# Optimization experiments

Hardware: AMD Instinct MI355X
Metric: run time of the kernel (lower is better)

## Reference

```python
import jax, jax.numpy as jnp
import numpy as np

M, K, D = 8, 4096, 128
N, H, W = 8, 64, 64


def setup_inputs() -> dict:
    key = jax.random.key(0)
    k1, k2, k3, k4 = jax.random.split(key, 4)
    codes = jax.random.randint(k1, (N, H, W, M), 0, K, dtype=jnp.int64)
    codebook = jax.random.normal(k2, (M, K, D), dtype=jnp.float32)
    wq = jax.random.normal(k3, (M, D, D), dtype=jnp.float32) / jnp.sqrt(jnp.float32(D))
    bq = jax.random.normal(k4, (M, D), dtype=jnp.float32) * 0.01
    return {"codes": codes, "codebook": codebook, "wq": wq, "bq": bq}


def reference(codes, codebook, wq, bq):
    n, h, w, m = codes.shape
    # gather: indexed[n,h,w,m,d] = codebook[m_idx, codes[n,h,w,m_idx]]
    ix = jnp.arange(m)  # broadcasts against codes' last dim
    indexed = codebook[ix, codes]  # [n,h,w,m,d]
    # per-group small matmul + bias
    out = jnp.einsum('nhwmd,mcd->nhwmc', indexed, wq) + bq  # [n,h,w,m,d]
    return out.reshape(n, h, w, -1).transpose(0, 3, 1, 2)  # [n, m*d, h, w]
```

## Files before the change

### kernel.cpp

```cpp
#include <hip/hip_runtime.h>
#include <hip/hip_bf16.h>

#define PM 8
#define PK 4096
#define PD 128
#define PN 8
#define PH 64
#define PW 64

typedef __attribute__((ext_vector_type(8))) short bf16x8;
typedef __attribute__((ext_vector_type(4))) float f32x4;
typedef __attribute__((ext_vector_type(8))) short short8v;

__device__ inline unsigned short f2bf_rne(float f) {
    unsigned int u = __float_as_uint(f);
    unsigned int r = (u + 0x7FFFu + ((u >> 16) & 1u)) >> 16;
    return (unsigned short)r;
}
__device__ inline float bf2f(unsigned short s) {
    return __uint_as_float(((unsigned int)s) << 16);
}

__device__ inline bf16x8 loadcvt8(const float* __restrict__ p) {
    f32x4 x0 = *(const f32x4*)p;
    f32x4 x1 = *(const f32x4*)(p + 4);
    bf16x8 r;
#pragma unroll
    for (int j = 0; j < 4; ++j) {
        r[j]     = (short)f2bf_rne(x0[j]);
        r[j + 4] = (short)f2bf_rne(x1[j]);
    }
    return r;
}

__global__ __launch_bounds__(256) void build_table(
        const float* __restrict__ codebook,
        const float* __restrict__ wq,
        const float* __restrict__ bq,
        unsigned short* __restrict__ table) {
    __shared__ unsigned short ldsA[2048 * 8];
    __shared__ float lds_bq[PD];
    const int b = blockIdx.x;
    const int m = b & 7;
    const int kt0 = (b >> 3) * 128;
    const int tid = threadIdx.x;
    const int wv = tid >> 6;
    const int l  = tid & 63;
    const int lr = l & 15;
    const int lg = l >> 4;

    const float* cb = codebook + (size_t)m * PK * PD;
    const float* wm = wq + (size_t)m * PD * PD;

    if (tid < PD) lds_bq[tid] = bq[m * PD + tid];

    {
        const int lr_s = tid & 15;
        const int u0 = (tid >> 4) * 8;
#pragma unroll
        for (int i = 0; i < 8; ++i) {
            const int u  = u0 + i;
            const int cs = u >> 4;
            const int kk = (u >> 2) & 3;
            const int lgs = u & 3;
            bf16x8 v = loadcvt8(wm + (size_t)(cs * 16 + lr_s) * PD + kk * 32 + lgs * 8);
            *(bf16x8*)&ldsA[(size_t)(u * 16 + lr_s) * 8] = v;
        }
    }

    bf16x8 bfragc[2][4];
#pragma unroll
    for (int ks = 0; ks < 2; ++ks) {
        const int k = kt0 + wv * 32 + ks * 16 + lr;
        const float* src = cb + (size_t)k * PD + lg * 8;
#pragma unroll
        for (int kk = 0; kk < 4; ++kk) {
            bfragc[ks][kk] = loadcvt8(src + kk * 32);
        }
    }
    __syncthreads();

#pragma unroll
    for (int cs = 0; cs < 8; ++cs) {
        bf16x8 afragw[4];
#pragma unroll
        for (int kk = 0; kk < 4; ++kk) {
            const int u = (cs << 4) | (kk << 2) | lg;
            afragw[kk] = *(const bf16x8*)&ldsA[(size_t)(u * 16 + lr) * 8];
        }
        const f32x4 bias4 = *(const f32x4*)&lds_bq[cs * 16 + lg * 4];
#pragma unroll
        for (int ks = 0; ks < 2; ++ks) {
            f32x4 acc = {0.f, 0.f, 0.f, 0.f};
#pragma unroll
            for (int kk = 0; kk < 4; ++kk) {
                acc = __builtin_amdgcn_mfma_f32_16x16x32_bf16(
                        afragw[kk], bfragc[ks][kk], acc, 0, 0, 0);
            }
            const int k = kt0 + wv * 32 + ks * 16 + lr;
            unsigned int p0 = (unsigned int)f2bf_rne(acc[0] + bias4[0])
                            | ((unsigned int)f2bf_rne(acc[1] + bias4[1]) << 16);
            unsigned int p1 = (unsigned int)f2bf_rne(acc[2] + bias4[2])
                            | ((unsigned int)f2bf_rne(acc[3] + bias4[3]) << 16);
            uint2 pk; pk.x = p0; pk.y = p1;
            *(uint2*)&table[((size_t)(m * PK + k)) * PD + cs * 16 + lg * 4] = pk;
        }
    }
}

__global__ __launch_bounds__(256) void gather_scatter(
        const int* __restrict__ codes,
        const unsigned short* __restrict__ table,
        float* __restrict__ out) {
    const int b = blockIdx.x;
    const int m = b & 7;
    const int rest = b >> 3;
    const int n = rest >> 6;
    const int h = rest & 63;
    const int tid = threadIdx.x;
    const int p   = tid >> 2;
    const int sub = tid & 3;

    const int code = codes[((n * PH + h) * PW + p) * PM + m];
    const unsigned short* row = table + ((size_t)m * PK + code) * PD;

    short8v v[4];
#pragma unroll
    for (int i = 0; i < 4; ++i) {
        v[i] = *(const short8v*)(row + i * 32 + sub * 8);
    }

    float* ob = out + (((size_t)n * (PM * PD) + m * PD + sub * 8) * PH + h) * PW + p;
#pragma unroll
    for (int i = 0; i < 4; ++i) {
#pragma unroll
        for (int j = 0; j < 8; ++j) {
            ob[(size_t)(i * 32 + j) * (PH * PW)] = bf2f((unsigned short)v[i][j]);
        }
    }
}

__global__ __launch_bounds__(256) void fused_direct(
        const int* __restrict__ codes,
        const float* __restrict__ codebook,
        const float* __restrict__ wq,
        const float* __restrict__ bq,
        float* __restrict__ out) {
    __shared__ float rows[PW][133];
    const int b = blockIdx.x;
    const int m = b & 7;
    const int rest = b >> 3;
    const int n = rest >> 6;
    const int h = rest & 63;
    const int tid = threadIdx.x;

    for (int idx = tid; idx < PW * 32; idx += 256) {
        const int r = idx >> 5;
        const int e = (idx & 31) * 4;
        const int code = codes[((n * PH + h) * PW + r) * PM + m];
        const float* src = codebook + ((size_t)m * PK + code) * PD + e;
#pragma unroll
        for (int j = 0; j < 4; ++j) rows[r][e + j] = src[j];
    }
    __syncthreads();

    const int w = tid & 63;
    const int cb0 = (tid >> 6) * 32;
    float* ob = out + (((size_t)n * (PM * PD) + m * PD + cb0) * PH + h) * PW + w;
    for (int ci = 0; ci < 32; ++ci) {
        const int c = cb0 + ci;
        const float* wr = wq + ((size_t)m * PD + c) * PD;
        float acc = bq[m * PD + c];
#pragma unroll 4
        for (int d = 0; d < PD; ++d) acc += rows[w][d] * wr[d];
        ob[(size_t)ci * (PH * PW)] = acc;
    }
}

extern "C" void kernel_launch(void* const* d_in, const int* in_sizes, int n_in,
                              void* d_out, int out_size, void* d_ws, size_t ws_size,
                              hipStream_t stream) {
    const int*   codes    = (const int*)  d_in[0];
    const float* codebook = (const float*)d_in[1];
    const float* wq       = (const float*)d_in[2];
    const float* bq       = (const float*)d_in[3];
    float* out = (float*)d_out;

    const size_t table_bytes = (size_t)PM * PK * PD * sizeof(unsigned short);
    if (ws_size >= table_bytes) {
        unsigned short* table = (unsigned short*)d_ws;
        build_table<<<dim3(256), dim3(256), 0, stream>>>(codebook, wq, bq, table);
        gather_scatter<<<dim3(PM * PN * PH), dim3(256), 0, stream>>>(codes, table, out);
    } else {
        fused_direct<<<dim3(PM * PN * PH), dim3(256), 0, stream>>>(codes, codebook, wq, bq, out);
    }
}
```

Baseline: 39.65 us.

## Transpose gathered table rows through LDS for vectorized coalesced output stores

Restructures the gather-scatter kernel so each block handles a 16-channel slice over 16 rows of h, gathering bf16 table chunks into LDS in a channel-major layout. The output is then written as 16-byte vector stores along w instead of scalar strided stores, which is meant to cut the cost of the scattered NCHW writes. This adds an LDS staging pass and a barrier. Each table row is now read in 32-byte pieces by separate blocks, and the codes array is re-read once per channel slice.

```diff
diff --git a/kernel.cpp b/kernel.cpp
--- a/kernel.cpp
+++ b/kernel.cpp
@@ -112,30 +112,64 @@
         const int* __restrict__ codes,
         const unsigned short* __restrict__ table,
         float* __restrict__ out) {
+    __shared__ unsigned int ldsW[8 * 16 * 64];
     const int b = blockIdx.x;
-    const int m = b & 7;
-    const int rest = b >> 3;
-    const int n = rest >> 6;
-    const int h = rest & 63;
+    const int m  = b & 7;
+    const int r  = b >> 3;
+    const int hg = r & 3;
+    const int cs = (r >> 2) & 7;
+    const int n  = r >> 5;
     const int tid = threadIdx.x;
-    const int p   = tid >> 2;
-    const int sub = tid & 3;
-
-    const int code = codes[((n * PH + h) * PW + p) * PM + m];
-    const unsigned short* row = table + ((size_t)m * PK + code) * PD;
-
-    short8v v[4];
-#pragma unroll
-    for (int i = 0; i < 4; ++i) {
-        v[i] = *(const short8v*)(row + i * 32 + sub * 8);
-    }
-
-    float* ob = out + (((size_t)n * (PM * PD) + m * PD + sub * 8) * PH + h) * PW + p;
-#pragma unroll
-    for (int i = 0; i < 4; ++i) {
-#pragma unroll
-        for (int j = 0; j < 8; ++j) {
-            ob[(size_t)(i * 32 + j) * (PH * PW)] = bf2f((unsigned short)v[i][j]);
+
+    {
+        const int w   = tid & 63;
+        const int hi2 = tid >> 6;
+#pragma unroll
+        for (int i = 0; i < 4; ++i) {
+            const int hl = hi2 * 4 + i;
+            const int h  = hg * 16 + hl;
+            const int code = codes[((size_t)((n * PH + h) * PW + w)) * PM + m];
+            const unsigned short* row =
+                table + ((size_t)m * PK + code) * PD + cs * 16;
+#pragma unroll
+            for (int q = 0; q < 2; ++q) {
+                uint4 ch = *(const uint4*)(row + q * 8);
+                ldsW[(q * 4 + 0) * 1024 + hl * 64 + w] = ch.x;
+                ldsW[(q * 4 + 1) * 1024 + hl * 64 + w] = ch.y;
+                ldsW[(q * 4 + 2) * 1024 + hl * 64 + w] = ch.z;
+                ldsW[(q * 4 + 3) * 1024 + hl * 64 + w] = ch.w;
+            }
+        }
+    }
+    __syncthreads();
+
+    const int v   = tid >> 6;
+    const int l   = tid & 63;
+    const int hl2 = l >> 4;
+    const int wq  = l & 15;
+#pragma unroll
+    for (int cpi = 0; cpi < 2; ++cpi) {
+        const int c2l = v * 2 + cpi;
+        const int cl0 = 2 * c2l;
+        float* p0 = out
+            + ((size_t)(n * (PM * PD) + m * PD + cs * 16 + cl0)) * (PH * PW)
+            + (hg * 16 + hl2) * PW + wq * 4;
+#pragma unroll
+        for (int hb = 0; hb < 4; ++hb) {
+            const int hl = hb * 4 + hl2;
+            uint4 ww = *(const uint4*)&ldsW[c2l * 1024 + hl * 64 + wq * 4];
+            f32x4 lo, hi;
+            lo[0] = __uint_as_float(ww.x << 16);
+            lo[1] = __uint_as_float(ww.y << 16);
+            lo[2] = __uint_as_float(ww.z << 16);
+            lo[3] = __uint_as_float(ww.w << 16);
+            hi[0] = __uint_as_float(ww.x & 0xFFFF0000u);
+            hi[1] = __uint_as_float(ww.y & 0xFFFF0000u);
+            hi[2] = __uint_as_float(ww.z & 0xFFFF0000u);
+            hi[3] = __uint_as_float(ww.w & 0xFFFF0000u);
+            float* pb = p0 + (size_t)hb * 4 * PW;
+            *(f32x4*)pb = lo;
+            *(f32x4*)(pb + (size_t)(PH * PW)) = hi;
         }
     }
 }
@@ -190,7 +224,7 @@
     if (ws_size >= table_bytes) {
         unsigned short* table = (unsigned short*)d_ws;
         build_table<<<dim3(256), dim3(256), 0, stream>>>(codebook, wq, bq, table);
-        gather_scatter<<<dim3(PM * PN * PH), dim3(256), 0, stream>>>(codes, table, out);
+        gather_scatter<<<dim3(2048), dim3(256), 0, stream>>>(codes, table, out);
     } else {
         fused_direct<<<dim3(PM * PN * PH), dim3(256), 0, stream>>>(codes, codebook, wq, bq, out);
     }
```

Result: no change. 40.42 us (+1.9%).
